# Kernel optimization log

Measured on AMD Instinct MI355X. Metric: run time of the kernel, lower is better.

Reference implementation:

```python
import jax, jax.numpy as jnp
import numpy as np

DIM = 1024
N_HEADS = 16
HEAD_DIM = DIM // N_HEADS


def setup_inputs() -> dict:
    key = jax.random.key(0)
    ks = jax.random.split(key, 6)
    s = DIM ** -0.5
    return {
        "x": jax.random.normal(ks[0], (2, 2048, DIM), dtype=jnp.float32),
        "Wq": jax.random.normal(ks[1], (DIM, DIM), dtype=jnp.float32) * s,
        "Wk": jax.random.normal(ks[2], (DIM, DIM), dtype=jnp.float32) * s,
        "Wv": jax.random.normal(ks[3], (DIM, DIM), dtype=jnp.float32) * s,
        "Wo": jax.random.normal(ks[4], (DIM, DIM), dtype=jnp.float32) * s,
        "bo": jax.random.normal(ks[5], (DIM,), dtype=jnp.float32) * 0.01,
    }


def reference(x, Wq, Wk, Wv, Wo, bo):
    B, T, C = x.shape
    H, D = N_HEADS, HEAD_DIM
    # Linear(dim, dim, bias=False): y = x @ W^T
    q = (x @ Wq.T).reshape(B, T, H, D).transpose(0, 2, 1, 3)  # B H T D
    k = (x @ Wk.T).reshape(B, T, H, D).transpose(0, 2, 1, 3)
    v = (x @ Wv.T).reshape(B, T, H, D).transpose(0, 2, 1, 3)
    q = q * (D ** -0.5)
    attn = jnp.einsum('bhqd,bhkd->bhqk', q, k)  # B H T T
    causal_mask = jnp.triu(jnp.ones((T, T), dtype=bool), k=1)
    attn = jnp.where(causal_mask, -jnp.inf, attn)
    attn = jax.nn.softmax(attn, axis=-1)
    out = jnp.einsum('bhqk,bhkd->bhqd', attn, v)  # B H T D
    out = out.transpose(0, 2, 1, 3).reshape(B, T, C)
    return out @ Wo.T + bo
```

## Files before the change

### kernel.cpp

```cpp
#include <hip/hip_runtime.h>
#include <math.h>

typedef __attribute__((ext_vector_type(8))) short bf16x8;
typedef __attribute__((ext_vector_type(4))) float f32x4;

__device__ __forceinline__ ushort f2bf(float f) {
  union { float f; unsigned u; } v; v.f = f;
  return (ushort)((v.u + 0x8000u) >> 16);
}

__device__ __forceinline__ void g2l16(const void* g, void* l) {
  __builtin_amdgcn_global_load_lds((const __attribute__((address_space(1))) unsigned*)g,
                                   (__attribute__((address_space(3))) unsigned*)l, 16, 0, 0);
}

__global__ __launch_bounds__(256) void cast_all(const float* __restrict__ x,
                                                const float* __restrict__ Wq,
                                                const float* __restrict__ Wk,
                                                const float* __restrict__ Wv,
                                                const float* __restrict__ Wo,
                                                ushort* __restrict__ xbf,
                                                ushort* __restrict__ wcat) {
  int i = blockIdx.x * 256 + threadIdx.x;
  if (i < 1048576) {
    float4 v = ((const float4*)x)[i];
    ushort4 u; u.x = f2bf(v.x); u.y = f2bf(v.y); u.z = f2bf(v.z); u.w = f2bf(v.w);
    ((ushort4*)xbf)[i] = u;
  } else {
    int j = i - 1048576;
    int sel = j >> 18;
    const float* src = (sel == 0) ? Wq : (sel == 1) ? Wk : (sel == 2) ? Wv : Wo;
    float scale = (sel == 0) ? 0.125f * 1.44269504088896f : 1.0f;
    float4 v = ((const float4*)src)[j & 0x3FFFF];
    ushort4 u;
    u.x = f2bf(v.x * scale); u.y = f2bf(v.y * scale);
    u.z = f2bf(v.z * scale); u.w = f2bf(v.w * scale);
    ((ushort4*)wcat)[j] = u;
  }
}

template<int BN, bool BF16_OUT, bool BIAS, bool SPLIT>
__global__ __launch_bounds__(256) void gemm_bt(const ushort* __restrict__ A,
                                               const ushort* __restrict__ B,
                                               void* __restrict__ Cout,
                                               const float* __restrict__ bias,
                                               int M, int N, int K) {
  __shared__ __align__(16) ushort As[2][128 * 32];
  __shared__ __align__(16) ushort Bs[2][BN * 32];
  const int m0 = blockIdx.y * 128, n0 = blockIdx.x * BN;
  const int tid = threadIdx.x, lane = tid & 63, wid = tid >> 6;
  const int quad = lane >> 4, lc = lane & 15;
  const int lrow = lane >> 2, lcol = (lane & 3) * 8;
  const int wm = (BN == 128) ? (wid >> 1) * 64 : wid * 32;
  const int wn = (BN == 128) ? (wid & 1) * 64 : 0;
  constexpr int MT = (BN == 128) ? 4 : 2;

  f32x4 acc[MT][4] = {};

  auto stage = [&](int k0, int nb) {
    const ushort* Ag = A + (size_t)(m0 + wid * 32 + lrow) * K + k0 + lcol;
    g2l16(Ag, &As[nb][wid * 1024]);
    g2l16(Ag + (size_t)16 * K, &As[nb][wid * 1024 + 512]);
    if constexpr (BN == 128) {
      const ushort* Bg = B + (size_t)(n0 + wid * 32 + lrow) * K + k0 + lcol;
      g2l16(Bg, &Bs[nb][wid * 1024]);
      g2l16(Bg + (size_t)16 * K, &Bs[nb][wid * 1024 + 512]);
    } else {
      const ushort* Bg = B + (size_t)(n0 + wid * 16 + lrow) * K + k0 + lcol;
      g2l16(Bg, &Bs[nb][wid * 512]);
    }
  };

  stage(0, 0);
  for (int k0 = 0; k0 < K; k0 += 32) {
    const int nb = (k0 >> 5) & 1;
    __syncthreads();
    if (k0 + 32 < K) stage(k0 + 32, nb ^ 1);

    bf16x8 af[MT], bfr[4];
#pragma unroll
    for (int t = 0; t < MT; t++)
      af[t] = *(const bf16x8*)&As[nb][(wm + t * 16 + lc) * 32 + quad * 8];
#pragma unroll
    for (int t = 0; t < 4; t++)
      bfr[t] = *(const bf16x8*)&Bs[nb][(wn + t * 16 + lc) * 32 + quad * 8];
#pragma unroll
    for (int mt = 0; mt < MT; mt++)
#pragma unroll
      for (int nt = 0; nt < 4; nt++)
        acc[mt][nt] = __builtin_amdgcn_mfma_f32_16x16x32_bf16(af[mt], bfr[nt], acc[mt][nt], 0, 0, 0);
  }

#pragma unroll
  for (int mt = 0; mt < MT; mt++) {
#pragma unroll
    for (int r = 0; r < 4; r++) {
      int row = m0 + wm + mt * 16 + quad * 4 + r;
#pragma unroll
      for (int nt = 0; nt < 4; nt++) {
        int col = n0 + wn + nt * 16 + lc;
        float v = acc[mt][nt][r];
        if (BIAS) v += bias[col];
        size_t dst;
        if (SPLIT) dst = ((size_t)(col >> 10) << 22) + (size_t)row * 1024 + (col & 1023);
        else       dst = (size_t)row * N + col;
        if (BF16_OUT) ((ushort*)Cout)[dst] = f2bf(v);
        else          ((float*)Cout)[dst]  = v;
      }
    }
  }
}

__global__ __launch_bounds__(256) void transpose_v(const ushort* __restrict__ Vb,
                                                   ushort* __restrict__ Vt) {
  __shared__ ushort tile[64][72];
  const int bh = blockIdx.y, b = bh >> 4, h = bh & 15;
  const int tt = blockIdx.x;
  const int tid = threadIdx.x;
#pragma unroll
  for (int i = 0; i < 2; i++) {
    int idx = i * 256 + tid;
    int trow = idx >> 3;
    int dcol = (idx & 7) * 8;
    uint4 v = *(const uint4*)(Vb + (size_t)(b * 2048 + tt * 64 + trow) * 1024 + h * 64 + dcol);
    ushort e[8]; *(uint4*)e = v;
#pragma unroll
    for (int j = 0; j < 8; j++) tile[dcol + j][trow] = e[j];
  }
  __syncthreads();
#pragma unroll
  for (int i = 0; i < 2; i++) {
    int idx = i * 256 + tid;
    int drow = idx >> 3;
    int tloc = (idx & 7) * 8;
    uint4 v = *(const uint4*)&tile[drow][tloc];
    *(uint4*)(Vt + (size_t)bh * 131072 + (size_t)drow * 2048 + tt * 64 + tloc) = v;
  }
}

__global__ __launch_bounds__(256, 6) void attn_kernel(const ushort* __restrict__ Qb,
                                                      const ushort* __restrict__ Kb,
                                                      const ushort* __restrict__ Vt,
                                                      float* __restrict__ O32,
                                                      float* __restrict__ L32) {
  __shared__ __align__(16) ushort Ks[2][64 * 32];
  __shared__ __align__(16) ushort Vs[2][64 * 32];
  __shared__ __align__(16) ushort Ps[4][16][72];

  const int bh = blockIdx.y, b = bh >> 4, h = bh & 15;
  const int f = 79 - (int)blockIdx.x;
  int qi, ci;
  if (f < 8)       { qi = f;                 ci = 0; }
  else if (f < 24) { int g = f - 8;  qi = 8  + (g >> 1); ci = g & 1; }
  else if (f < 48) { int g = f - 24; int q3 = g / 3; qi = 16 + q3; ci = g - 3 * q3; }
  else             { int g = f - 48; qi = 24 + (g >> 2); ci = g & 3; }

  const int t0 = ci * 8;
  const int t1 = min(t0 + 8, qi + 1);
  const int qb_block = qi * 64;

  const int tid = threadIdx.x, lane = tid & 63, wid = tid >> 6;
  const int quad = lane >> 4, lc = lane & 15;
  const int lrow = lane >> 2, lcol = (lane & 3) * 8;
  const int qbw = qb_block + wid * 16;

  const size_t kbase = (size_t)(b * 2048) * 1024 + h * 64;
  const size_t vbase = (size_t)bh * 131072;

  const ushort* Qp = Qb + kbase + (size_t)(qbw + lc) * 1024;
  bf16x8 qf0 = *(const bf16x8*)(Qp + quad * 8);
  bf16x8 qf1 = *(const bf16x8*)(Qp + 32 + quad * 8);

  f32x4 o_acc[4] = {};
  float l_r[4] = {0.f, 0.f, 0.f, 0.f};

  for (int kt = t0; kt < t1; kt++) {
    const int kb = kt * 64;
    __syncthreads();
#pragma unroll
    for (int cc = 0; cc < 2; cc++) {
      int ck = wid + cc * 4;
      int half = ck >> 2, rg = ck & 3;
      const ushort* gK = Kb + kbase + (size_t)(kb + rg * 16 + lrow) * 1024 + half * 32 + lcol;
      g2l16(gK, &Ks[half][rg * 512]);
      const ushort* gV = Vt + vbase + (size_t)(rg * 16 + lrow) * 2048 + kb + half * 32 + lcol;
      g2l16(gV, &Vs[half][rg * 512]);
    }
    __syncthreads();

    const bool diag = (kb + 63 > qbw);
#pragma unroll
    for (int c = 0; c < 4; c++) {
      bf16x8 kf0 = *(const bf16x8*)&Ks[0][(c * 16 + lc) * 32 + quad * 8];
      bf16x8 kf1 = *(const bf16x8*)&Ks[1][(c * 16 + lc) * 32 + quad * 8];
      f32x4 z = {};
      z = __builtin_amdgcn_mfma_f32_16x16x32_bf16(qf0, kf0, z, 0, 0, 0);
      z = __builtin_amdgcn_mfma_f32_16x16x32_bf16(qf1, kf1, z, 0, 0, 0);
#pragma unroll
      for (int r = 0; r < 4; r++) {
        float sv = z[r];
        if (diag && (kb + c * 16 + lc > qbw + quad * 4 + r)) sv = -1e30f;
        float pv = __builtin_amdgcn_exp2f(sv);
        l_r[r] += pv;
        Ps[wid][quad * 4 + r][c * 16 + lc] = f2bf(pv);
      }
    }
    __asm__ volatile("s_waitcnt lgkmcnt(0)" ::: "memory");
    bf16x8 ap0 = *(const bf16x8*)&Ps[wid][lc][quad * 8];
    bf16x8 ap1 = *(const bf16x8*)&Ps[wid][lc][32 + quad * 8];

#pragma unroll
    for (int nt = 0; nt < 4; nt++) {
      bf16x8 vb0 = *(const bf16x8*)&Vs[0][(nt * 16 + lc) * 32 + quad * 8];
      bf16x8 vb1 = *(const bf16x8*)&Vs[1][(nt * 16 + lc) * 32 + quad * 8];
      o_acc[nt] = __builtin_amdgcn_mfma_f32_16x16x32_bf16(ap0, vb0, o_acc[nt], 0, 0, 0);
      o_acc[nt] = __builtin_amdgcn_mfma_f32_16x16x32_bf16(ap1, vb1, o_acc[nt], 0, 0, 0);
    }
  }

#pragma unroll
  for (int r = 0; r < 4; r++) {
    float s_ = l_r[r];
    s_ += __shfl_xor(s_, 1);
    s_ += __shfl_xor(s_, 2);
    s_ += __shfl_xor(s_, 4);
    s_ += __shfl_xor(s_, 8);
    l_r[r] = s_;
  }
  if (lc == 0) {
#pragma unroll
    for (int r = 0; r < 4; r++)
      atomicAdd(&L32[(size_t)bh * 2048 + qbw + quad * 4 + r], l_r[r]);
  }
#pragma unroll
  for (int r = 0; r < 4; r++) {
    size_t orow = ((size_t)(b * 2048) + qbw + quad * 4 + r) * 1024 + h * 64 + lc;
#pragma unroll
    for (int nt = 0; nt < 4; nt++)
      atomicAdd(&O32[orow + nt * 16], o_acc[nt][r]);
  }
}

__global__ __launch_bounds__(256) void normalize_kernel(const float* __restrict__ O32,
                                                        const float* __restrict__ L32,
                                                        ushort* __restrict__ Out) {
  const int row = blockIdx.x;
  const int tid = threadIdx.x;
  const int col = tid * 4;
  const int b = row >> 11, t = row & 2047, h = col >> 6;
  const float inv = 1.0f / L32[(size_t)(b * 16 + h) * 2048 + t];
  float4 o = ((const float4*)(O32 + (size_t)row * 1024))[tid];
  ushort4 u;
  u.x = f2bf(o.x * inv); u.y = f2bf(o.y * inv);
  u.z = f2bf(o.z * inv); u.w = f2bf(o.w * inv);
  ((ushort4*)(Out + (size_t)row * 1024))[tid] = u;
}

extern "C" void kernel_launch(void* const* d_in, const int* in_sizes, int n_in,
                              void* d_out, int out_size, void* d_ws, size_t ws_size,
                              hipStream_t stream) {
  const float* x  = (const float*)d_in[0];
  const float* Wq = (const float*)d_in[1];
  const float* Wk = (const float*)d_in[2];
  const float* Wv = (const float*)d_in[3];
  const float* Wo = (const float*)d_in[4];
  const float* bo = (const float*)d_in[5];
  float* out = (float*)d_out;

  char* ws = (char*)d_ws;
  ushort* xbf  = (ushort*)(ws);
  ushort* wcat = (ushort*)(ws + (8ull  << 20));
  ushort* qkv  = (ushort*)(ws + (16ull << 20));
  ushort* Vt   = (ushort*)(ws);
  ushort* Qp   = qkv;
  ushort* Kp   = qkv + (1ull << 22);
  ushort* Vp   = qkv + (2ull << 22);
  float*  L32  = (float*)Vp;
  float*  O32  = out;
  ushort* attn_out = Qp;

  cast_all<<<8192, 256, 0, stream>>>(x, Wq, Wk, Wv, Wo, xbf, wcat);

  gemm_bt<128, true, false, true><<<dim3(24, 32), 256, 0, stream>>>(
      xbf, wcat, qkv, nullptr, 4096, 3072, 1024);

  transpose_v<<<dim3(32, 32), 256, 0, stream>>>(Vp, Vt);

  hipMemsetAsync(O32, 0, (size_t)4096 * 1024 * 4, stream);
  hipMemsetAsync(L32, 0, (size_t)32 * 2048 * 4, stream);

  attn_kernel<<<dim3(80, 32), 256, 0, stream>>>(Qp, Kp, Vt, O32, L32);

  normalize_kernel<<<4096, 256, 0, stream>>>(O32, L32, attn_out);

  gemm_bt<64, false, true, false><<<dim3(16, 32), 256, 0, stream>>>(
      attn_out, wcat + (size_t)3072 * 1024, out, bo, 4096, 1024, 1024);
}
```

Baseline: 212.4 us.

## Fuse V transpose into QKV GEMM epilogue and deepen output-projection K tiling

The QKV GEMM now writes the V columns directly in transposed per-head layout, which removes the separate transpose_v kernel launch and its extra read and write of V. The output projection becomes a dedicated kernel that stages 64-wide K slices (two 32-wide subtiles) per sync, with a 2x2 wave layout instead of 4x1. The transposed V stores are strided scatters (stride 2048 elements), so that epilogue may write less efficiently. Workspace aliasing moves Vt into the qkv region and L32 to the start of the workspace.

```diff
diff --git a/kernel.cpp b/kernel.cpp
--- a/kernel.cpp
+++ b/kernel.cpp
@@ -39,36 +39,28 @@
   }
 }
 
-template<int BN, bool BF16_OUT, bool BIAS, bool SPLIT>
-__global__ __launch_bounds__(256) void gemm_bt(const ushort* __restrict__ A,
-                                               const ushort* __restrict__ B,
-                                               void* __restrict__ Cout,
-                                               const float* __restrict__ bias,
-                                               int M, int N, int K) {
+__global__ __launch_bounds__(256) void gemm_qkv(const ushort* __restrict__ A,
+                                                const ushort* __restrict__ B,
+                                                ushort* __restrict__ QK,
+                                                ushort* __restrict__ Vt) {
+  const int K = 1024;
   __shared__ __align__(16) ushort As[2][128 * 32];
-  __shared__ __align__(16) ushort Bs[2][BN * 32];
-  const int m0 = blockIdx.y * 128, n0 = blockIdx.x * BN;
+  __shared__ __align__(16) ushort Bs[2][128 * 32];
+  const int m0 = blockIdx.y * 128, n0 = blockIdx.x * 128;
   const int tid = threadIdx.x, lane = tid & 63, wid = tid >> 6;
   const int quad = lane >> 4, lc = lane & 15;
   const int lrow = lane >> 2, lcol = (lane & 3) * 8;
-  const int wm = (BN == 128) ? (wid >> 1) * 64 : wid * 32;
-  const int wn = (BN == 128) ? (wid & 1) * 64 : 0;
-  constexpr int MT = (BN == 128) ? 4 : 2;
-
-  f32x4 acc[MT][4] = {};
+  const int wm = (wid >> 1) * 64, wn = (wid & 1) * 64;
+
+  f32x4 acc[4][4] = {};
 
   auto stage = [&](int k0, int nb) {
     const ushort* Ag = A + (size_t)(m0 + wid * 32 + lrow) * K + k0 + lcol;
     g2l16(Ag, &As[nb][wid * 1024]);
     g2l16(Ag + (size_t)16 * K, &As[nb][wid * 1024 + 512]);
-    if constexpr (BN == 128) {
-      const ushort* Bg = B + (size_t)(n0 + wid * 32 + lrow) * K + k0 + lcol;
-      g2l16(Bg, &Bs[nb][wid * 1024]);
-      g2l16(Bg + (size_t)16 * K, &Bs[nb][wid * 1024 + 512]);
-    } else {
-      const ushort* Bg = B + (size_t)(n0 + wid * 16 + lrow) * K + k0 + lcol;
-      g2l16(Bg, &Bs[nb][wid * 512]);
-    }
+    const ushort* Bg = B + (size_t)(n0 + wid * 32 + lrow) * K + k0 + lcol;
+    g2l16(Bg, &Bs[nb][wid * 1024]);
+    g2l16(Bg + (size_t)16 * K, &Bs[nb][wid * 1024 + 512]);
   };
 
   stage(0, 0);
@@ -77,64 +69,102 @@
     __syncthreads();
     if (k0 + 32 < K) stage(k0 + 32, nb ^ 1);
 
-    bf16x8 af[MT], bfr[4];
-#pragma unroll
-    for (int t = 0; t < MT; t++)
+    bf16x8 af[4], bfr[4];
+#pragma unroll
+    for (int t = 0; t < 4; t++)
       af[t] = *(const bf16x8*)&As[nb][(wm + t * 16 + lc) * 32 + quad * 8];
 #pragma unroll
     for (int t = 0; t < 4; t++)
       bfr[t] = *(const bf16x8*)&Bs[nb][(wn + t * 16 + lc) * 32 + quad * 8];
 #pragma unroll
-    for (int mt = 0; mt < MT; mt++)
+    for (int mt = 0; mt < 4; mt++)
 #pragma unroll
       for (int nt = 0; nt < 4; nt++)
         acc[mt][nt] = __builtin_amdgcn_mfma_f32_16x16x32_bf16(af[mt], bfr[nt], acc[mt][nt], 0, 0, 0);
   }
 
-#pragma unroll
-  for (int mt = 0; mt < MT; mt++) {
+  const int sel = n0 >> 10;
+#pragma unroll
+  for (int mt = 0; mt < 4; mt++) {
 #pragma unroll
     for (int r = 0; r < 4; r++) {
       int row = m0 + wm + mt * 16 + quad * 4 + r;
 #pragma unroll
       for (int nt = 0; nt < 4; nt++) {
         int col = n0 + wn + nt * 16 + lc;
-        float v = acc[mt][nt][r];
-        if (BIAS) v += bias[col];
-        size_t dst;
-        if (SPLIT) dst = ((size_t)(col >> 10) << 22) + (size_t)row * 1024 + (col & 1023);
-        else       dst = (size_t)row * N + col;
-        if (BF16_OUT) ((ushort*)Cout)[dst] = f2bf(v);
-        else          ((float*)Cout)[dst]  = v;
+        ushort v = f2bf(acc[mt][nt][r]);
+        if (sel < 2) {
+          QK[((size_t)sel << 22) + (size_t)row * 1024 + (col & 1023)] = v;
+        } else {
+          int hd = col & 1023;
+          size_t bh = (size_t)((row >> 11) * 16 + (hd >> 6));
+          Vt[bh * 131072 + (size_t)(hd & 63) * 2048 + (row & 2047)] = v;
+        }
       }
     }
   }
 }
 
-__global__ __launch_bounds__(256) void transpose_v(const ushort* __restrict__ Vb,
-                                                   ushort* __restrict__ Vt) {
-  __shared__ ushort tile[64][72];
-  const int bh = blockIdx.y, b = bh >> 4, h = bh & 15;
-  const int tt = blockIdx.x;
-  const int tid = threadIdx.x;
-#pragma unroll
-  for (int i = 0; i < 2; i++) {
-    int idx = i * 256 + tid;
-    int trow = idx >> 3;
-    int dcol = (idx & 7) * 8;
-    uint4 v = *(const uint4*)(Vb + (size_t)(b * 2048 + tt * 64 + trow) * 1024 + h * 64 + dcol);
-    ushort e[8]; *(uint4*)e = v;
-#pragma unroll
-    for (int j = 0; j < 8; j++) tile[dcol + j][trow] = e[j];
-  }
-  __syncthreads();
-#pragma unroll
-  for (int i = 0; i < 2; i++) {
-    int idx = i * 256 + tid;
-    int drow = idx >> 3;
-    int tloc = (idx & 7) * 8;
-    uint4 v = *(const uint4*)&tile[drow][tloc];
-    *(uint4*)(Vt + (size_t)bh * 131072 + (size_t)drow * 2048 + tt * 64 + tloc) = v;
+__global__ __launch_bounds__(256) void gemm_proj(const ushort* __restrict__ A,
+                                                 const ushort* __restrict__ B,
+                                                 float* __restrict__ C,
+                                                 const float* __restrict__ bias) {
+  const int K = 1024;
+  __shared__ __align__(16) ushort As[2][2][128 * 32];
+  __shared__ __align__(16) ushort Bs[2][2][64 * 32];
+  const int m0 = blockIdx.y * 128, n0 = blockIdx.x * 64;
+  const int tid = threadIdx.x, lane = tid & 63, wid = tid >> 6;
+  const int quad = lane >> 4, lc = lane & 15;
+  const int lrow = lane >> 2, lcol = (lane & 3) * 8;
+  const int wm = (wid >> 1) * 64, wn = (wid & 1) * 32;
+
+  f32x4 acc[4][2] = {};
+
+  auto stage = [&](int k0, int nb) {
+    const ushort* Ag = A + (size_t)(m0 + wid * 32 + lrow) * K + k0 + lcol;
+    g2l16(Ag,                      &As[nb][0][wid * 1024]);
+    g2l16(Ag + (size_t)16 * K,     &As[nb][0][wid * 1024 + 512]);
+    g2l16(Ag + 32,                 &As[nb][1][wid * 1024]);
+    g2l16(Ag + (size_t)16 * K + 32, &As[nb][1][wid * 1024 + 512]);
+    const ushort* Bg = B + (size_t)(n0 + wid * 16 + lrow) * K + k0 + lcol;
+    g2l16(Bg,      &Bs[nb][0][wid * 512]);
+    g2l16(Bg + 32, &Bs[nb][1][wid * 512]);
+  };
+
+  stage(0, 0);
+  for (int k0 = 0; k0 < K; k0 += 64) {
+    const int nb = (k0 >> 6) & 1;
+    __syncthreads();
+    if (k0 + 64 < K) stage(k0 + 64, nb ^ 1);
+
+#pragma unroll
+    for (int ks = 0; ks < 2; ks++) {
+      bf16x8 af[4], bfr[2];
+#pragma unroll
+      for (int t = 0; t < 4; t++)
+        af[t] = *(const bf16x8*)&As[nb][ks][(wm + t * 16 + lc) * 32 + quad * 8];
+#pragma unroll
+      for (int t = 0; t < 2; t++)
+        bfr[t] = *(const bf16x8*)&Bs[nb][ks][(wn + t * 16 + lc) * 32 + quad * 8];
+#pragma unroll
+      for (int mt = 0; mt < 4; mt++)
+#pragma unroll
+        for (int nt = 0; nt < 2; nt++)
+          acc[mt][nt] = __builtin_amdgcn_mfma_f32_16x16x32_bf16(af[mt], bfr[nt], acc[mt][nt], 0, 0, 0);
+    }
+  }
+
+#pragma unroll
+  for (int mt = 0; mt < 4; mt++) {
+#pragma unroll
+    for (int r = 0; r < 4; r++) {
+      int row = m0 + wm + mt * 16 + quad * 4 + r;
+#pragma unroll
+      for (int nt = 0; nt < 2; nt++) {
+        int col = n0 + wn + nt * 16 + lc;
+        C[(size_t)row * 1024 + col] = acc[mt][nt][r] + bias[col];
+      }
+    }
   }
 }
 
@@ -271,28 +301,24 @@
   ushort* xbf  = (ushort*)(ws);
   ushort* wcat = (ushort*)(ws + (8ull  << 20));
   ushort* qkv  = (ushort*)(ws + (16ull << 20));
-  ushort* Vt   = (ushort*)(ws);
   ushort* Qp   = qkv;
   ushort* Kp   = qkv + (1ull << 22);
-  ushort* Vp   = qkv + (2ull << 22);
-  float*  L32  = (float*)Vp;
+  ushort* Vt   = qkv + (2ull << 22);
+  float*  L32  = (float*)ws;
   float*  O32  = out;
   ushort* attn_out = Qp;
 
   cast_all<<<8192, 256, 0, stream>>>(x, Wq, Wk, Wv, Wo, xbf, wcat);
 
-  gemm_bt<128, true, false, true><<<dim3(24, 32), 256, 0, stream>>>(
-      xbf, wcat, qkv, nullptr, 4096, 3072, 1024);
-
-  transpose_v<<<dim3(32, 32), 256, 0, stream>>>(Vp, Vt);
-
+  gemm_qkv<<<dim3(24, 32), 256, 0, stream>>>(xbf, wcat, qkv, Vt);
+
+  hipMemsetAsync(L32, 0, (size_t)32 * 2048 * 4, stream);
   hipMemsetAsync(O32, 0, (size_t)4096 * 1024 * 4, stream);
-  hipMemsetAsync(L32, 0, (size_t)32 * 2048 * 4, stream);
 
   attn_kernel<<<dim3(80, 32), 256, 0, stream>>>(Qp, Kp, Vt, O32, L32);
 
   normalize_kernel<<<4096, 256, 0, stream>>>(O32, L32, attn_out);
 
-  gemm_bt<64, false, true, false><<<dim3(16, 32), 256, 0, stream>>>(
-      attn_out, wcat + (size_t)3072 * 1024, out, bo, 4096, 1024, 1024);
-}
+  gemm_proj<<<dim3(16, 32), 256, 0, stream>>>(
+      attn_out, wcat + (size_t)3072 * 1024, out, bo);
+}
```

New measurement: 215.9 us. About the same (+1.7%).
